# Kernel optimization log

Measured on AMD Instinct MI355X. Metric: run time of the kernel, lower is better.

The kernel has to match this reference:

```python
import jax, jax.numpy as jnp
import numpy as np

SCALE = 8.0  # sqrt(hid=64), passed as init arg `scale`


def setup_inputs() -> dict:
    key = jax.random.key(0)
    kq, kk, kv, km = jax.random.split(key, 4)
    B, S, H = 32, 2048, 64  # B = bs*n_head
    q = jax.random.normal(kq, (B, S, H), dtype=jnp.float32)
    k = jax.random.normal(kk, (B, S, H), dtype=jnp.float32)
    v = jax.random.normal(kv, (B, S, H), dtype=jnp.float32)
    mask = jax.random.bernoulli(km, 0.1, (B, S, S))  # True = masked out
    return {"q": q, "k": k, "v": v, "mask": mask, "cca": 0}


def reference(q, k, v, mask, cca):
    # scores: [B, Sq, Sk]
    attn = jnp.einsum('bqh,bkh->bqk', q, k) / SCALE
    if mask is not None:
        attn = jnp.where(mask, jnp.finfo(q.dtype).min, attn)
    if cca:
        # CCA branch: softmax over the query/sequence axis (dim=1)
        attn = jax.nn.softmax(attn, axis=1)
        ctx = jnp.einsum('bq,bkh->bqh', attn.squeeze(-1)[..., None].squeeze(-1), v) if attn.ndim == 2 else jnp.einsum('bqk,bkh->bqh', attn, v)
    else:
        attn = jax.nn.softmax(attn, axis=2)
        ctx = jnp.einsum('bqk,bkh->bqh', attn, v)  # [B, Sq, H]
    return (ctx, attn)
```

## Files before the change

kernel.cpp:

```cpp
#include <hip/hip_runtime.h>
#include <hip/hip_bf16.h>

typedef __bf16    bf16x8_t __attribute__((ext_vector_type(8)));
typedef float     f32x4_t  __attribute__((ext_vector_type(4)));
typedef short     s16x4_t  __attribute__((ext_vector_type(4)));
typedef short     s16x8_t  __attribute__((ext_vector_type(8)));
typedef unsigned  u32x4_t  __attribute__((ext_vector_type(4)));

#define S_LEN 2048
#define HDIM  64
#define BQ    32
#define NTHREADS 512
#define PSTR_B 4112
#define BMSTR 264

__device__ __forceinline__ short f2bf(float f) {
    return __builtin_bit_cast(short, (__bf16)f);
}
__device__ __forceinline__ float bf2f(short s) {
    return __builtin_bit_cast(float, ((unsigned)(unsigned short)s) << 16);
}
__device__ __forceinline__ short* pelem(short* P, int row, int e) {
    return (short*)((char*)P + (unsigned)row * PSTR_B + (unsigned)e * 2u);
}
__device__ __forceinline__ const short* pelemc(const short* P, int row, int e) {
    return pelem(const_cast<short*>(P), row, e);
}
__device__ __forceinline__ unsigned nzmask16(u32x4_t w) {
    unsigned n = 0;
    #pragma unroll
    for (int i = 0; i < 4; ++i) {
        const unsigned x = w[i];
        const unsigned t = (x & 0x7F7F7F7Fu) + 0x7F7F7F7Fu;
        const unsigned z = ((t | x) & 0x80808080u) >> 7;
        n |= ((z * 0x10204081u) >> 28) << (4 * i);
    }
    return n;
}
__device__ __forceinline__ unsigned nzmask4w(u32x4_t w) {
    return (w[0] ? 1u : 0u) | (w[1] ? 2u : 0u) | (w[2] ? 4u : 0u) | (w[3] ? 8u : 0u);
}

#define PK8(lo, hi, out8) { s16x8_t _t; \
    _t[0]=f2bf((lo)[0]); _t[1]=f2bf((lo)[1]); _t[2]=f2bf((lo)[2]); _t[3]=f2bf((lo)[3]); \
    _t[4]=f2bf((hi)[0]); _t[5]=f2bf((hi)[1]); _t[6]=f2bf((hi)[2]); _t[7]=f2bf((hi)[3]); \
    (out8) = __builtin_bit_cast(bf16x8_t, _t); }
#define PKV(src, dst) { s16x8_t _t; \
    _t[0]=f2bf((src)[0]); _t[1]=f2bf((src)[1]); _t[2]=f2bf((src)[2]); _t[3]=f2bf((src)[3]); \
    _t[4]=f2bf((src)[4]); _t[5]=f2bf((src)[5]); _t[6]=f2bf((src)[6]); _t[7]=f2bf((src)[7]); \
    (dst) = __builtin_bit_cast(bf16x8_t, _t); }

__global__ void detect_mask(const unsigned char* __restrict__ M, int* __restrict__ flags) {
    __shared__ int cnt[4];
    if (threadIdx.x < 4) cnt[threadIdx.x] = 0;
    __syncthreads();
    int local[4] = {0, 0, 0, 0};
    for (int i = threadIdx.x; i < 16384; i += 256)
        if (M[i]) local[i & 3]++;
    #pragma unroll
    for (int c = 0; c < 4; ++c)
        if (local[c]) atomicAdd(&cnt[c], local[c]);
    __syncthreads();
    if (threadIdx.x == 0) {
        int stride;
        if (cnt[1] == 0 && cnt[2] == 0 && cnt[3] == 0)      stride = 4;
        else if (cnt[0] == 0 && cnt[1] == 0)                stride = 4;
        else                                                stride = 1;
        flags[0] = stride;
    }
}

__global__ __launch_bounds__(NTHREADS, 2)
void sdpa_one(const float* __restrict__ Q, const float* __restrict__ K,
              const float* __restrict__ V, const unsigned char* __restrict__ M,
              const int* __restrict__ MF, float* __restrict__ OUT)
{
    __shared__ short Plds[BQ * (PSTR_B / 2)];
    __shared__ unsigned char Bm[BQ * BMSTR];
    __shared__ float Pvp[4][BQ][17];
    __shared__ float rowsum[BQ];
    __shared__ float rinv_s[BQ];

    const int tid  = threadIdx.x;
    const int w    = tid >> 6;
    const int lane = tid & 63;
    const int col  = lane & 15;
    const int kg   = lane >> 4;
    const int mstride = MF[0];

    const int id   = blockIdx.x;
    const int slot = id >> 3;
    const int b    = ((slot >> 6) << 3) | (id & 7);
    const int q0   = (slot & 63) * BQ;

    float* attn_out = OUT + (size_t)32 * S_LEN * HDIM;

    if (tid < BQ) rowsum[tid] = 0.f;

    {
        const int row  = tid >> 4;
        const int segE = (tid & 15) * 128;
        unsigned long long bits[2] = {0ull, 0ull};
        if (mstride == 1) {
            const unsigned char* mp = M + (size_t)b * S_LEN * S_LEN
                                        + (size_t)(q0 + row) * S_LEN + segE;
            #pragma unroll
            for (int j = 0; j < 8; ++j)
                bits[j >> 2] |= (unsigned long long)nzmask16(*(const u32x4_t*)(mp + j * 16))
                                << (16 * (j & 3));
        } else {
            const unsigned* mp = (const unsigned*)M + (size_t)b * S_LEN * S_LEN
                                   + (size_t)(q0 + row) * S_LEN + segE;
            #pragma unroll
            for (int j = 0; j < 32; ++j)
                bits[j >> 4] |= (unsigned long long)nzmask4w(*(const u32x4_t*)(mp + j * 4))
                                << (4 * (j & 15));
        }
        unsigned long long* bp = (unsigned long long*)&Bm[row * BMSTR + (tid & 15) * 16];
        bp[0] = bits[0]; bp[1] = bits[1];
    }

    bf16x8_t af[2][2];
    #pragma unroll
    for (int m = 0; m < 2; ++m)
        #pragma unroll
        for (int kk = 0; kk < 2; ++kk) {
            const float* qp = Q + ((size_t)b * S_LEN + q0 + m * 16 + col) * HDIM + kk * 32 + kg * 8;
            const f32x4_t qa = *(const f32x4_t*)qp;
            const f32x4_t qb = *(const f32x4_t*)(qp + 4);
            PK8(qa, qb, af[m][kk]);
        }
    __syncthreads();

    float rs[2][4] = {{0.f,0.f,0.f,0.f},{0.f,0.f,0.f,0.f}};
    {
        const float* Kb = K + (size_t)b * S_LEN * HDIM;
        f32x4_t A0,B0,C0,D0, A1,B1,C1,D1;
#define LDK(f, AX,BX,CX,DX) { \
    const float* kp = Kb + (size_t)(w * 256 + (f) * 16 + col) * HDIM + kg * 8; \
    AX = *(const f32x4_t*)kp;        BX = *(const f32x4_t*)(kp + 4); \
    CX = *(const f32x4_t*)(kp + 32); DX = *(const f32x4_t*)(kp + 36); }
#define STEP(f, AX,BX,CX,DX, PF, fp) { \
    bf16x8_t kb0, kb1; PK8(AX, BX, kb0); PK8(CX, DX, kb1); \
    if (PF) LDK(fp, AX,BX,CX,DX); \
    f32x4_t acc0 = {0.f,0.f,0.f,0.f}, acc1 = {0.f,0.f,0.f,0.f}; \
    acc0 = __builtin_amdgcn_mfma_f32_16x16x32_bf16(af[0][0], kb0, acc0, 0,0,0); \
    acc0 = __builtin_amdgcn_mfma_f32_16x16x32_bf16(af[0][1], kb1, acc0, 0,0,0); \
    acc1 = __builtin_amdgcn_mfma_f32_16x16x32_bf16(af[1][0], kb0, acc1, 0,0,0); \
    acc1 = __builtin_amdgcn_mfma_f32_16x16x32_bf16(af[1][1], kb1, acc1, 0,0,0); \
    const int c = w * 256 + (f) * 16 + col; \
    _Pragma("unroll") \
    for (int r = 0; r < 4; ++r) { \
        const int row0 = kg * 4 + r; \
        const unsigned b0m = Bm[row0 * BMSTR + (c >> 3)]; \
        const float p0 = ((b0m >> (c & 7)) & 1u) ? 0.f : __expf(acc0[r] * 0.125f); \
        rs[0][r] += p0; \
        *pelem(Plds, row0, c) = f2bf(p0); \
        const int row1 = 16 + kg * 4 + r; \
        const unsigned b1m = Bm[row1 * BMSTR + (c >> 3)]; \
        const float p1 = ((b1m >> (c & 7)) & 1u) ? 0.f : __expf(acc1[r] * 0.125f); \
        rs[1][r] += p1; \
        *pelem(Plds, row1, c) = f2bf(p1); \
    } }
        LDK(0, A0,B0,C0,D0);
        LDK(1, A1,B1,C1,D1);
        #pragma unroll
        for (int ff = 0; ff < 16; ff += 2) {
            STEP(ff,     A0,B0,C0,D0, (ff + 2 < 16), ff + 2);
            STEP(ff + 1, A1,B1,C1,D1, (ff + 3 < 16), ff + 3);
        }
#undef LDK
#undef STEP
    }
    #pragma unroll
    for (int m = 0; m < 2; ++m)
        #pragma unroll
        for (int r = 0; r < 4; ++r) {
            float s = rs[m][r];
            s += __shfl_xor(s, 1); s += __shfl_xor(s, 2);
            s += __shfl_xor(s, 4); s += __shfl_xor(s, 8);
            if (col == 0) atomicAdd(&rowsum[m * 16 + kg * 4 + r], s);
        }
    __syncthreads();
    if (tid < BQ) rinv_s[tid] = 1.0f / rowsum[tid];
    __syncthreads();

    const int hb    = (w & 3) * 16;
    const int kbase = (w >> 2) * 1024;
    const float* Vb = V + (size_t)b * S_LEN * HDIM;

    const int srow = w * 4 + (lane >> 4);
    const float my_rinv = rinv_s[srow];
    float* abp = attn_out + ((size_t)b * S_LEN + q0 + srow) * S_LEN + (lane & 15) * 4;

    f32x4_t cacc0 = {0.f,0.f,0.f,0.f}, cacc1 = {0.f,0.f,0.f,0.f};
    float vr0[8], vr1[8];
#define LOADV(kc, dst) { \
    const float* vp = Vb + (size_t)(kbase + (kc) * 32 + kg * 8) * HDIM + hb + col; \
    dst[0] = vp[0];        dst[1] = vp[HDIM];     dst[2] = vp[2*HDIM]; dst[3] = vp[3*HDIM]; \
    dst[4] = vp[4*HDIM];   dst[5] = vp[5*HDIM];   dst[6] = vp[6*HDIM]; dst[7] = vp[7*HDIM]; }
#define PVSTEP(kc, vsrc) { \
    bf16x8_t vbf; PKV(vsrc, vbf); \
    const int ke = kbase + (kc) * 32 + kg * 8; \
    const bf16x8_t pa0 = *(const bf16x8_t*)pelemc(Plds, col,      ke); \
    const bf16x8_t pa1 = *(const bf16x8_t*)pelemc(Plds, 16 + col, ke); \
    cacc0 = __builtin_amdgcn_mfma_f32_16x16x32_bf16(pa0, vbf, cacc0, 0,0,0); \
    cacc1 = __builtin_amdgcn_mfma_f32_16x16x32_bf16(pa1, vbf, cacc1, 0,0,0); }
#define BURST(s) { _Pragma("unroll") for (int c4 = 0; c4 < 4; ++c4) { \
    const int cb = (s) * 256 + c4 * 64 + (lane & 15) * 4; \
    const s16x4_t pv = *(const s16x4_t*)pelemc(Plds, srow, cb); \
    f32x4_t o; \
    o[0] = bf2f(pv[0]) * my_rinv; o[1] = bf2f(pv[1]) * my_rinv; \
    o[2] = bf2f(pv[2]) * my_rinv; o[3] = bf2f(pv[3]) * my_rinv; \
    *(f32x4_t*)(abp + (s) * 256 + c4 * 64) = o; } }

    LOADV(0, vr0);
    #pragma unroll
    for (int kc2 = 0; kc2 < 16; ++kc2) {
        LOADV(2 * kc2 + 1, vr1);
        if ((kc2 & 1) == 0) BURST(kc2 >> 1);
        PVSTEP(2 * kc2, vr0);
        if (kc2 < 15) LOADV(2 * kc2 + 2, vr0);
        PVSTEP(2 * kc2 + 1, vr1);
    }
#undef LOADV
#undef PVSTEP
#undef BURST

    if (w >= 4) {
        #pragma unroll
        for (int r = 0; r < 4; ++r) {
            Pvp[w - 4][kg * 4 + r][col]      = cacc0[r];
            Pvp[w - 4][16 + kg * 4 + r][col] = cacc1[r];
        }
    }
    __syncthreads();
    if (w < 4) {
        #pragma unroll
        for (int r = 0; r < 4; ++r) {
            const int row0 = kg * 4 + r;
            const int row1 = 16 + kg * 4 + r;
            OUT[((size_t)b * S_LEN + q0 + row0) * HDIM + hb + col]
                = (cacc0[r] + Pvp[w][row0][col]) * rinv_s[row0];
            OUT[((size_t)b * S_LEN + q0 + row1) * HDIM + hb + col]
                = (cacc1[r] + Pvp[w][row1][col]) * rinv_s[row1];
        }
    }
}

extern "C" void kernel_launch(void* const* d_in, const int* in_sizes, int n_in,
                              void* d_out, int out_size, void* d_ws, size_t ws_size,
                              hipStream_t stream)
{
    const float* q = (const float*)d_in[0];
    const float* k = (const float*)d_in[1];
    const float* v = (const float*)d_in[2];
    const unsigned char* mask = (const unsigned char*)d_in[3];
    int* mflags = (int*)d_ws;
    float* out = (float*)d_out;
    detect_mask<<<dim3(1), dim3(256), 0, stream>>>(mask, mflags);
    sdpa_one<<<dim3(2048), dim3(NTHREADS), 0, stream>>>(q, k, v, mask, mflags, out);
}
```

Before: 441.3 us.

## Halve query tile to 16 rows and double blocks per CU

Cuts the per-block query tile from 32 to 16 rows, which halves the shared-memory P buffer and the register accumulators. The kernel now launches twice as many blocks and raises the launch-bounds occupancy hint from 2 to 4 blocks per CU. The PV loop is re-pipelined with four V prefetch buffers, and the attention-matrix write bursts are reshaped for 32-lane rows. In exchange, K and V are now re-read from global memory twice as often per batch, and each MFMA step does half as much work per K/V load.

```diff
diff --git a/kernel.cpp b/kernel.cpp
--- a/kernel.cpp
+++ b/kernel.cpp
@@ -9,7 +9,7 @@
 
 #define S_LEN 2048
 #define HDIM  64
-#define BQ    32
+#define BQ    16
 #define NTHREADS 512
 #define PSTR_B 4112
 #define BMSTR 264
@@ -70,7 +70,7 @@
     }
 }
 
-__global__ __launch_bounds__(NTHREADS, 2)
+__global__ __launch_bounds__(NTHREADS, 4)
 void sdpa_one(const float* __restrict__ Q, const float* __restrict__ K,
               const float* __restrict__ V, const unsigned char* __restrict__ M,
               const int* __restrict__ MF, float* __restrict__ OUT)
@@ -90,49 +90,46 @@
 
     const int id   = blockIdx.x;
     const int slot = id >> 3;
-    const int b    = ((slot >> 6) << 3) | (id & 7);
-    const int q0   = (slot & 63) * BQ;
+    const int b    = ((slot >> 7) << 3) | (id & 7);
+    const int q0   = (slot & 127) * BQ;
 
     float* attn_out = OUT + (size_t)32 * S_LEN * HDIM;
 
     if (tid < BQ) rowsum[tid] = 0.f;
 
     {
-        const int row  = tid >> 4;
-        const int segE = (tid & 15) * 128;
-        unsigned long long bits[2] = {0ull, 0ull};
+        const int row  = tid >> 5;
+        const int segE = (tid & 31) * 64;
+        unsigned long long bits = 0ull;
         if (mstride == 1) {
             const unsigned char* mp = M + (size_t)b * S_LEN * S_LEN
                                         + (size_t)(q0 + row) * S_LEN + segE;
             #pragma unroll
-            for (int j = 0; j < 8; ++j)
-                bits[j >> 2] |= (unsigned long long)nzmask16(*(const u32x4_t*)(mp + j * 16))
-                                << (16 * (j & 3));
+            for (int j = 0; j < 4; ++j)
+                bits |= (unsigned long long)nzmask16(*(const u32x4_t*)(mp + j * 16))
+                        << (16 * j);
         } else {
             const unsigned* mp = (const unsigned*)M + (size_t)b * S_LEN * S_LEN
                                    + (size_t)(q0 + row) * S_LEN + segE;
             #pragma unroll
-            for (int j = 0; j < 32; ++j)
-                bits[j >> 4] |= (unsigned long long)nzmask4w(*(const u32x4_t*)(mp + j * 4))
-                                << (4 * (j & 15));
+            for (int j = 0; j < 16; ++j)
+                bits |= (unsigned long long)nzmask4w(*(const u32x4_t*)(mp + j * 4))
+                        << (4 * j);
         }
-        unsigned long long* bp = (unsigned long long*)&Bm[row * BMSTR + (tid & 15) * 16];
-        bp[0] = bits[0]; bp[1] = bits[1];
-    }
-
-    bf16x8_t af[2][2];
-    #pragma unroll
-    for (int m = 0; m < 2; ++m)
-        #pragma unroll
-        for (int kk = 0; kk < 2; ++kk) {
-            const float* qp = Q + ((size_t)b * S_LEN + q0 + m * 16 + col) * HDIM + kk * 32 + kg * 8;
-            const f32x4_t qa = *(const f32x4_t*)qp;
-            const f32x4_t qb = *(const f32x4_t*)(qp + 4);
-            PK8(qa, qb, af[m][kk]);
-        }
-    __syncthreads();
-
-    float rs[2][4] = {{0.f,0.f,0.f,0.f},{0.f,0.f,0.f,0.f}};
+        *(unsigned long long*)&Bm[row * BMSTR + (segE >> 3)] = bits;
+    }
+
+    bf16x8_t af[2];
+    #pragma unroll
+    for (int kk = 0; kk < 2; ++kk) {
+        const float* qp = Q + ((size_t)b * S_LEN + q0 + col) * HDIM + kk * 32 + kg * 8;
+        const f32x4_t qa = *(const f32x4_t*)qp;
+        const f32x4_t qb = *(const f32x4_t*)(qp + 4);
+        PK8(qa, qb, af[kk]);
+    }
+    __syncthreads();
+
+    float rs[4] = {0.f, 0.f, 0.f, 0.f};
     {
         const float* Kb = K + (size_t)b * S_LEN * HDIM;
         f32x4_t A0,B0,C0,D0, A1,B1,C1,D1;
@@ -143,24 +140,17 @@
 #define STEP(f, AX,BX,CX,DX, PF, fp) { \
     bf16x8_t kb0, kb1; PK8(AX, BX, kb0); PK8(CX, DX, kb1); \
     if (PF) LDK(fp, AX,BX,CX,DX); \
-    f32x4_t acc0 = {0.f,0.f,0.f,0.f}, acc1 = {0.f,0.f,0.f,0.f}; \
-    acc0 = __builtin_amdgcn_mfma_f32_16x16x32_bf16(af[0][0], kb0, acc0, 0,0,0); \
-    acc0 = __builtin_amdgcn_mfma_f32_16x16x32_bf16(af[0][1], kb1, acc0, 0,0,0); \
-    acc1 = __builtin_amdgcn_mfma_f32_16x16x32_bf16(af[1][0], kb0, acc1, 0,0,0); \
-    acc1 = __builtin_amdgcn_mfma_f32_16x16x32_bf16(af[1][1], kb1, acc1, 0,0,0); \
+    f32x4_t acc = {0.f,0.f,0.f,0.f}; \
+    acc = __builtin_amdgcn_mfma_f32_16x16x32_bf16(af[0], kb0, acc, 0,0,0); \
+    acc = __builtin_amdgcn_mfma_f32_16x16x32_bf16(af[1], kb1, acc, 0,0,0); \
     const int c = w * 256 + (f) * 16 + col; \
     _Pragma("unroll") \
     for (int r = 0; r < 4; ++r) { \
         const int row0 = kg * 4 + r; \
         const unsigned b0m = Bm[row0 * BMSTR + (c >> 3)]; \
-        const float p0 = ((b0m >> (c & 7)) & 1u) ? 0.f : __expf(acc0[r] * 0.125f); \
-        rs[0][r] += p0; \
+        const float p0 = ((b0m >> (c & 7)) & 1u) ? 0.f : __expf(acc[r] * 0.125f); \
+        rs[r] += p0; \
         *pelem(Plds, row0, c) = f2bf(p0); \
-        const int row1 = 16 + kg * 4 + r; \
-        const unsigned b1m = Bm[row1 * BMSTR + (c >> 3)]; \
-        const float p1 = ((b1m >> (c & 7)) & 1u) ? 0.f : __expf(acc1[r] * 0.125f); \
-        rs[1][r] += p1; \
-        *pelem(Plds, row1, c) = f2bf(p1); \
     } }
         LDK(0, A0,B0,C0,D0);
         LDK(1, A1,B1,C1,D1);
@@ -173,14 +163,12 @@
 #undef STEP
     }
     #pragma unroll
-    for (int m = 0; m < 2; ++m)
-        #pragma unroll
-        for (int r = 0; r < 4; ++r) {
-            float s = rs[m][r];
-            s += __shfl_xor(s, 1); s += __shfl_xor(s, 2);
-            s += __shfl_xor(s, 4); s += __shfl_xor(s, 8);
-            if (col == 0) atomicAdd(&rowsum[m * 16 + kg * 4 + r], s);
-        }
+    for (int r = 0; r < 4; ++r) {
+        float s = rs[r];
+        s += __shfl_xor(s, 1); s += __shfl_xor(s, 2);
+        s += __shfl_xor(s, 4); s += __shfl_xor(s, 8);
+        if (col == 0) atomicAdd(&rowsum[kg * 4 + r], s);
+    }
     __syncthreads();
     if (tid < BQ) rinv_s[tid] = 1.0f / rowsum[tid];
     __syncthreads();
@@ -189,39 +177,37 @@
     const int kbase = (w >> 2) * 1024;
     const float* Vb = V + (size_t)b * S_LEN * HDIM;
 
-    const int srow = w * 4 + (lane >> 4);
+    const int srow = w * 2 + (lane >> 5);
     const float my_rinv = rinv_s[srow];
-    float* abp = attn_out + ((size_t)b * S_LEN + q0 + srow) * S_LEN + (lane & 15) * 4;
-
-    f32x4_t cacc0 = {0.f,0.f,0.f,0.f}, cacc1 = {0.f,0.f,0.f,0.f};
-    float vr0[8], vr1[8];
+    float* abp = attn_out + ((size_t)b * S_LEN + q0 + srow) * S_LEN + (lane & 31) * 4;
+
+    f32x4_t cacc = {0.f, 0.f, 0.f, 0.f};
+    float vr0[8], vr1[8], vr2[8], vr3[8];
 #define LOADV(kc, dst) { \
     const float* vp = Vb + (size_t)(kbase + (kc) * 32 + kg * 8) * HDIM + hb + col; \
     dst[0] = vp[0];        dst[1] = vp[HDIM];     dst[2] = vp[2*HDIM]; dst[3] = vp[3*HDIM]; \
     dst[4] = vp[4*HDIM];   dst[5] = vp[5*HDIM];   dst[6] = vp[6*HDIM]; dst[7] = vp[7*HDIM]; }
 #define PVSTEP(kc, vsrc) { \
     bf16x8_t vbf; PKV(vsrc, vbf); \
-    const int ke = kbase + (kc) * 32 + kg * 8; \
-    const bf16x8_t pa0 = *(const bf16x8_t*)pelemc(Plds, col,      ke); \
-    const bf16x8_t pa1 = *(const bf16x8_t*)pelemc(Plds, 16 + col, ke); \
-    cacc0 = __builtin_amdgcn_mfma_f32_16x16x32_bf16(pa0, vbf, cacc0, 0,0,0); \
-    cacc1 = __builtin_amdgcn_mfma_f32_16x16x32_bf16(pa1, vbf, cacc1, 0,0,0); }
-#define BURST(s) { _Pragma("unroll") for (int c4 = 0; c4 < 4; ++c4) { \
-    const int cb = (s) * 256 + c4 * 64 + (lane & 15) * 4; \
+    const bf16x8_t pa = *(const bf16x8_t*)pelemc(Plds, col, kbase + (kc) * 32 + kg * 8); \
+    cacc = __builtin_amdgcn_mfma_f32_16x16x32_bf16(pa, vbf, cacc, 0,0,0); }
+#define BURST(sec) { \
+    const int cb = (sec) * 128 + (lane & 31) * 4; \
     const s16x4_t pv = *(const s16x4_t*)pelemc(Plds, srow, cb); \
     f32x4_t o; \
     o[0] = bf2f(pv[0]) * my_rinv; o[1] = bf2f(pv[1]) * my_rinv; \
     o[2] = bf2f(pv[2]) * my_rinv; o[3] = bf2f(pv[3]) * my_rinv; \
-    *(f32x4_t*)(abp + (s) * 256 + c4 * 64) = o; } }
-
-    LOADV(0, vr0);
-    #pragma unroll
-    for (int kc2 = 0; kc2 < 16; ++kc2) {
-        LOADV(2 * kc2 + 1, vr1);
-        if ((kc2 & 1) == 0) BURST(kc2 >> 1);
-        PVSTEP(2 * kc2, vr0);
-        if (kc2 < 15) LOADV(2 * kc2 + 2, vr0);
-        PVSTEP(2 * kc2 + 1, vr1);
+    *(f32x4_t*)(abp + (sec) * 128) = o; }
+
+    LOADV(0, vr0); LOADV(1, vr1); LOADV(2, vr2); LOADV(3, vr3);
+    #pragma unroll
+    for (int g = 0; g < 8; ++g) {
+        BURST(2 * g);
+        PVSTEP(4 * g, vr0);     if (4 * g + 4 < 32) LOADV(4 * g + 4, vr0);
+        PVSTEP(4 * g + 1, vr1); if (4 * g + 5 < 32) LOADV(4 * g + 5, vr1);
+        BURST(2 * g + 1);
+        PVSTEP(4 * g + 2, vr2); if (4 * g + 6 < 32) LOADV(4 * g + 6, vr2);
+        PVSTEP(4 * g + 3, vr3); if (4 * g + 7 < 32) LOADV(4 * g + 7, vr3);
     }
 #undef LOADV
 #undef PVSTEP
@@ -229,21 +215,16 @@
 
     if (w >= 4) {
         #pragma unroll
-        for (int r = 0; r < 4; ++r) {
-            Pvp[w - 4][kg * 4 + r][col]      = cacc0[r];
-            Pvp[w - 4][16 + kg * 4 + r][col] = cacc1[r];
-        }
+        for (int r = 0; r < 4; ++r)
+            Pvp[w - 4][kg * 4 + r][col] = cacc[r];
     }
     __syncthreads();
     if (w < 4) {
         #pragma unroll
         for (int r = 0; r < 4; ++r) {
-            const int row0 = kg * 4 + r;
-            const int row1 = 16 + kg * 4 + r;
-            OUT[((size_t)b * S_LEN + q0 + row0) * HDIM + hb + col]
-                = (cacc0[r] + Pvp[w][row0][col]) * rinv_s[row0];
-            OUT[((size_t)b * S_LEN + q0 + row1) * HDIM + hb + col]
-                = (cacc1[r] + Pvp[w][row1][col]) * rinv_s[row1];
+            const int row = kg * 4 + r;
+            OUT[((size_t)b * S_LEN + q0 + row) * HDIM + hb + col]
+                = (cacc[r] + Pvp[w][row][col]) * rinv_s[row];
         }
     }
 }
@@ -259,5 +240,5 @@
     int* mflags = (int*)d_ws;
     float* out = (float*)d_out;
     detect_mask<<<dim3(1), dim3(256), 0, stream>>>(mask, mflags);
-    sdpa_one<<<dim3(2048), dim3(NTHREADS), 0, stream>>>(q, k, v, mask, mflags, out);
-}
+    sdpa_one<<<dim3(4096), dim3(NTHREADS), 0, stream>>>(q, k, v, mask, mflags, out);
+}
```

Result: slower. 511.2 us (+15.9%).

## Deepen V prefetch to four buffers and move attn write after PV loop

Applied to the files above, without the earlier changes.

The PV loop now keeps four V register buffers in flight instead of two, so more global loads can be outstanding while the MFMAs run. The normalized attention-probability write-out, which used to be interleaved with the PV steps, now runs as a separate loop after the PV accumulation. The intent is to reduce stalls on V loads and to stop the large attn stores from competing with the V loads. In exchange it uses more VGPRs, which may lower occupancy, and the attn stores no longer overlap with the PV compute.

```diff
diff --git a/kernel.cpp b/kernel.cpp
--- a/kernel.cpp
+++ b/kernel.cpp
@@ -189,12 +189,9 @@
     const int kbase = (w >> 2) * 1024;
     const float* Vb = V + (size_t)b * S_LEN * HDIM;
 
-    const int srow = w * 4 + (lane >> 4);
-    const float my_rinv = rinv_s[srow];
-    float* abp = attn_out + ((size_t)b * S_LEN + q0 + srow) * S_LEN + (lane & 15) * 4;
-
     f32x4_t cacc0 = {0.f,0.f,0.f,0.f}, cacc1 = {0.f,0.f,0.f,0.f};
-    float vr0[8], vr1[8];
+    {
+        float vr0[8], vr1[8], vr2[8], vr3[8];
 #define LOADV(kc, dst) { \
     const float* vp = Vb + (size_t)(kbase + (kc) * 32 + kg * 8) * HDIM + hb + col; \
     dst[0] = vp[0];        dst[1] = vp[HDIM];     dst[2] = vp[2*HDIM]; dst[3] = vp[3*HDIM]; \
@@ -206,26 +203,31 @@
     const bf16x8_t pa1 = *(const bf16x8_t*)pelemc(Plds, 16 + col, ke); \
     cacc0 = __builtin_amdgcn_mfma_f32_16x16x32_bf16(pa0, vbf, cacc0, 0,0,0); \
     cacc1 = __builtin_amdgcn_mfma_f32_16x16x32_bf16(pa1, vbf, cacc1, 0,0,0); }
-#define BURST(s) { _Pragma("unroll") for (int c4 = 0; c4 < 4; ++c4) { \
-    const int cb = (s) * 256 + c4 * 64 + (lane & 15) * 4; \
-    const s16x4_t pv = *(const s16x4_t*)pelemc(Plds, srow, cb); \
-    f32x4_t o; \
-    o[0] = bf2f(pv[0]) * my_rinv; o[1] = bf2f(pv[1]) * my_rinv; \
-    o[2] = bf2f(pv[2]) * my_rinv; o[3] = bf2f(pv[3]) * my_rinv; \
-    *(f32x4_t*)(abp + (s) * 256 + c4 * 64) = o; } }
-
-    LOADV(0, vr0);
-    #pragma unroll
-    for (int kc2 = 0; kc2 < 16; ++kc2) {
-        LOADV(2 * kc2 + 1, vr1);
-        if ((kc2 & 1) == 0) BURST(kc2 >> 1);
-        PVSTEP(2 * kc2, vr0);
-        if (kc2 < 15) LOADV(2 * kc2 + 2, vr0);
-        PVSTEP(2 * kc2 + 1, vr1);
-    }
+        LOADV(0, vr0); LOADV(1, vr1); LOADV(2, vr2); LOADV(3, vr3);
+        #pragma unroll
+        for (int g = 0; g < 8; ++g) {
+            PVSTEP(4 * g,     vr0); if (4 * g + 4 < 32) LOADV(4 * g + 4, vr0);
+            PVSTEP(4 * g + 1, vr1); if (4 * g + 5 < 32) LOADV(4 * g + 5, vr1);
+            PVSTEP(4 * g + 2, vr2); if (4 * g + 6 < 32) LOADV(4 * g + 6, vr2);
+            PVSTEP(4 * g + 3, vr3); if (4 * g + 7 < 32) LOADV(4 * g + 7, vr3);
+        }
 #undef LOADV
 #undef PVSTEP
-#undef BURST
+    }
+
+    {
+        const int srow = w * 4 + kg;
+        const float my_rinv = rinv_s[srow];
+        float* abp = attn_out + ((size_t)b * S_LEN + q0 + srow) * S_LEN + col * 4;
+        #pragma unroll 4
+        for (int sec = 0; sec < 32; ++sec) {
+            const s16x4_t pv = *(const s16x4_t*)pelemc(Plds, srow, sec * 64 + col * 4);
+            f32x4_t o;
+            o[0] = bf2f(pv[0]) * my_rinv; o[1] = bf2f(pv[1]) * my_rinv;
+            o[2] = bf2f(pv[2]) * my_rinv; o[3] = bf2f(pv[3]) * my_rinv;
+            *(f32x4_t*)(abp + sec * 64) = o;
+        }
+    }
 
     if (w >= 4) {
         #pragma unroll
```

After: 444.9 us. No clear change (+0.8%).
